# Performance work log

Measured on AMD Instinct MI355X. Metric: run time of the kernel, lower is better.

## Reference

```python
import jax, jax.numpy as jnp
import numpy as np

B, S, D = 1, 4096, 512
H, DK, DV = 8, 64, 64


def setup_inputs() -> dict:
    key = jax.random.key(0)
    ks = jax.random.split(key, 8)
    s = 1.0 / np.sqrt(D)
    return {
        "queries": jax.random.normal(ks[0], (B, S, D), jnp.float32),
        "keys": jax.random.normal(ks[1], (B, S, D), jnp.float32),
        "values": jax.random.normal(ks[2], (B, S, D), jnp.float32),
        # Linear weights stored as [in, out] for x @ W
        "Wq": jax.random.normal(ks[3], (D, H * DK), jnp.float32) * s,
        "Wk": jax.random.normal(ks[4], (D, H * DK), jnp.float32) * s,
        "Wv": jax.random.normal(ks[5], (D, H * DV), jnp.float32) * s,
        "Wo": jax.random.normal(ks[6], (H * DV, D), jnp.float32) * s,
        "bo": jax.random.normal(ks[7], (D,), jnp.float32) * 0.02,
    }


def reference(queries, keys, values, Wq, Wk, Wv, Wo, bo):
    b, qlen = values.shape[0], queries.shape[1]
    q = (queries @ Wq).reshape(b, qlen, H, DK)
    k = (keys @ Wk).reshape(b, keys.shape[1], H, DK)
    v = (values @ Wv).reshape(b, values.shape[1], H, DV)
    scale = DK ** 0.5
    # naive full attention: materialize [b, h, sq, sk] scores
    scores = jnp.einsum("bqhd,bkhd->bhqk", q, k) / scale
    attn = jax.nn.softmax(scores, axis=-1)
    out = jnp.einsum("bhqk,bkhd->bqhd", attn, v).reshape(b, qlen, H * DV)
    out = out @ Wo + bo          # first fc_out
    out = out @ Wo + bo          # second fc_out (module applies it twice when not reversible)
    return out
```

## Files before the change

kernel.cpp:

```cpp
#include <hip/hip_runtime.h>

#define S_LEN  4096
#define DMODEL 512
#define NH     8
#define HD     64

typedef _Float16 f16x8 __attribute__((ext_vector_type(8)));
typedef _Float16 f16x4 __attribute__((ext_vector_type(4)));
typedef float    f32x4 __attribute__((ext_vector_type(4)));

static __device__ __forceinline__ unsigned short f2h(float x) {
  return __builtin_bit_cast(unsigned short, (_Float16)x);
}

__global__ __launch_bounds__(256) void wtrans_kernel(
    const float* __restrict__ w0, const float* __restrict__ w1,
    const float* __restrict__ w2, const float* __restrict__ w3,
    unsigned short* __restrict__ o0, unsigned short* __restrict__ o1,
    unsigned short* __restrict__ o2, unsigned short* __restrict__ o3,
    unsigned short* __restrict__ o3s)
{
  __shared__ unsigned short T[64 * 72];
  const float* W; unsigned short* O;
  switch (blockIdx.z) {
    case 0:  W = w0; O = o0; break;
    case 1:  W = w1; O = o1; break;
    case 2:  W = w2; O = o2; break;
    default: W = w3; O = o3; break;
  }
  const int tid = threadIdx.x;
  const int k0 = blockIdx.x * 64, n0 = blockIdx.y * 64;
  const int c4 = (tid & 15) * 4;
#pragma unroll
  for (int rp = 0; rp < 4; ++rp) {
    int r = rp * 16 + (tid >> 4);
    float4 x = *(const float4*)(W + (k0 + r) * DMODEL + n0 + c4);
    T[(c4 + 0) * 72 + r] = f2h(x.x);
    T[(c4 + 1) * 72 + r] = f2h(x.y);
    T[(c4 + 2) * 72 + r] = f2h(x.z);
    T[(c4 + 3) * 72 + r] = f2h(x.w);
    if (blockIdx.z == 3) {
      f16x4 st;
      st[0] = (_Float16)x.x; st[1] = (_Float16)x.y;
      st[2] = (_Float16)x.z; st[3] = (_Float16)x.w;
      *(f16x4*)&o3s[(k0 + r) * DMODEL + n0 + c4] = st;
    }
  }
  __syncthreads();
#pragma unroll
  for (int it = 0; it < 2; ++it) {
    int i = tid + it * 256;
    int nl = i >> 3, c = i & 7;
    *(f16x8*)&O[(n0 + nl) * DMODEL + k0 + c * 8] = *(const f16x8*)&T[nl * 72 + c * 8];
  }
}

__global__ __launch_bounds__(64) void bo2_kernel(
    const float* __restrict__ Wo, const float* __restrict__ bo,
    float* __restrict__ bo2)
{
  int col = blockIdx.x * 64 + threadIdx.x;
  float s = bo[col];
#pragma unroll 8
  for (int j = 0; j < DMODEL; ++j) s = fmaf(bo[j], Wo[j * DMODEL + col], s);
  bo2[col] = s;
}

__global__ __launch_bounds__(256) void gemm_kernel(
    const void* __restrict__ A0, const void* __restrict__ A1,
    const void* __restrict__ A2, const void* __restrict__ A3,
    const unsigned short* __restrict__ B0, const unsigned short* __restrict__ B1,
    const unsigned short* __restrict__ B2, const unsigned short* __restrict__ B3,
    void* __restrict__ C0, void* __restrict__ C1,
    void* __restrict__ C2, void* __restrict__ C3,
    const float* __restrict__ bias, unsigned short* __restrict__ vtg,
    int a_fp32_mask, int c_fp32_mask)
{
  constexpr int K = DMODEL, N = DMODEL;
  __shared__ unsigned short As[64 * 32];
  __shared__ unsigned short Bs[64 * 32];
  const int z = blockIdx.z;
  if (z == 3 && blockIdx.x >= 8) return;
  const void* Av; const unsigned short* Bt; void* Cv;
  switch (z) {
    case 0:  Av = A0; Bt = B0; Cv = C0; break;
    case 1:  Av = A1; Bt = B1; Cv = C1; break;
    case 2:  Av = A2; Bt = B2; Cv = C2; break;
    default: Av = A3; Bt = B3; Cv = C3; break;
  }
  const int a_fp32 = (a_fp32_mask >> z) & 1;
  const int c_fp32 = (c_fp32_mask >> z) & 1;
  const int tid  = threadIdx.x;
  const int lane = tid & 63;
  const int wid  = tid >> 6;
  const int quad = lane >> 4, l16 = lane & 15;
  const int m0 = blockIdx.x * 64, n0 = blockIdx.y * 64;
  const int wm = (wid >> 1) * 32, wn = (wid & 1) * 32;
  const int r  = tid >> 2, ck = (tid & 3) * 8;
  f32x4 acc[2][2] = {};

  for (int k0 = 0; k0 < K; k0 += 32) {
    __syncthreads();
    if (a_fp32) {
      const float* p = (const float*)Av + (m0 + r) * K + k0 + ck;
      float4 x = *(const float4*)p;
      float4 y = *(const float4*)(p + 4);
      f16x8 av;
      av[0] = (_Float16)x.x; av[1] = (_Float16)x.y;
      av[2] = (_Float16)x.z; av[3] = (_Float16)x.w;
      av[4] = (_Float16)y.x; av[5] = (_Float16)y.y;
      av[6] = (_Float16)y.z; av[7] = (_Float16)y.w;
      *(f16x8*)&As[r * 32 + ck] = av;
    } else {
      *(f16x8*)&As[r * 32 + ck] =
          *(const f16x8*)((const unsigned short*)Av + (m0 + r) * K + k0 + ck);
    }
    *(f16x8*)&Bs[r * 32 + ck] = *(const f16x8*)(Bt + (n0 + r) * K + k0 + ck);
    __syncthreads();

    f16x8 a0 = *(const f16x8*)&As[(wm + l16) * 32 + quad * 8];
    f16x8 a1 = *(const f16x8*)&As[(wm + 16 + l16) * 32 + quad * 8];
    f16x8 b0 = *(const f16x8*)&Bs[(wn + l16) * 32 + quad * 8];
    f16x8 b1 = *(const f16x8*)&Bs[(wn + 16 + l16) * 32 + quad * 8];
    acc[0][0] = __builtin_amdgcn_mfma_f32_16x16x32_f16(a0, b0, acc[0][0], 0, 0, 0);
    acc[0][1] = __builtin_amdgcn_mfma_f32_16x16x32_f16(a0, b1, acc[0][1], 0, 0, 0);
    acc[1][0] = __builtin_amdgcn_mfma_f32_16x16x32_f16(a1, b0, acc[1][0], 0, 0, 0);
    acc[1][1] = __builtin_amdgcn_mfma_f32_16x16x32_f16(a1, b1, acc[1][1], 0, 0, 0);
  }

  const int do_vt = (vtg != nullptr) && (z == 2);
#pragma unroll
  for (int mt = 0; mt < 2; ++mt)
#pragma unroll
    for (int nt = 0; nt < 2; ++nt) {
      int col = n0 + wn + nt * 16 + l16;
      float bv = bias ? bias[col] : 0.f;
#pragma unroll
      for (int g = 0; g < 4; ++g) {
        int row = m0 + wm + mt * 16 + quad * 4 + g;
        float val = acc[mt][nt][g] + bv;
        if (do_vt)        vtg[col * S_LEN + row] = f2h(val);
        else if (c_fp32)  ((float*)Cv)[row * N + col] = val;
        else              ((unsigned short*)Cv)[row * N + col] = f2h(val);
      }
    }
}

__global__ __launch_bounds__(512) void attn_kernel(
    const unsigned short* __restrict__ Qb, const unsigned short* __restrict__ Kb,
    const unsigned short* __restrict__ VtG, unsigned short* __restrict__ Ob)
{
  __shared__ unsigned short Ks[2][64 * 72];
  __shared__ unsigned short Vt[2][64 * 72];
  __shared__ _Float16 Osc[4][64][16];
  __shared__ float    Msc[4][16];
  __shared__ float    Lsc[4][16];

  const int tid  = threadIdx.x;
  const int lane = tid & 63;
  const int wid  = tid >> 6;
  const int qsub = wid & 3;
  const int kh   = wid >> 2;
  const int quad = lane >> 4, l16 = lane & 15;
  const int qb = blockIdx.x, h = blockIdx.y;
  const int hc = h * HD;

  const int qrow = qb * 64 + qsub * 16 + l16;
  const f16x8 bq0 = *(const f16x8*)(Qb + qrow * DMODEL + hc + quad * 8);
  const f16x8 bq1 = *(const f16x8*)(Qb + qrow * DMODEL + hc + 32 + quad * 8);

  f32x4 o[4] = {};
  float m_run = -1e30f, l_run = 0.f;

  for (int kbi = 0; kbi < 32; ++kbi) {
    __syncthreads();
#pragma unroll
    for (int it = 0; it < 2; ++it) {
      int s = it * 512 + tid;
      int khs = s >> 9, n = (s >> 3) & 63, c = s & 7;
      int key = khs * 2048 + kbi * 64 + n;
      *(f16x8*)&Ks[khs][n * 72 + c * 8] =
          *(const f16x8*)(Kb + key * DMODEL + hc + c * 8);
      *(f16x8*)&Vt[khs][n * 72 + c * 8] =
          *(const f16x8*)(VtG + (hc + n) * S_LEN + khs * 2048 + kbi * 64 + c * 8);
    }
    __syncthreads();

    f32x4 sT[4];
#pragma unroll
    for (int kt = 0; kt < 4; ++kt) {
      f32x4 a = {};
      f16x8 ak0 = *(const f16x8*)&Ks[kh][(kt * 16 + l16) * 72 + quad * 8];
      f16x8 ak1 = *(const f16x8*)&Ks[kh][(kt * 16 + l16) * 72 + 32 + quad * 8];
      a = __builtin_amdgcn_mfma_f32_16x16x32_f16(ak0, bq0, a, 0, 0, 0);
      a = __builtin_amdgcn_mfma_f32_16x16x32_f16(ak1, bq1, a, 0, 0, 0);
      sT[kt] = a;
    }

    float vmax = -1e30f;
#pragma unroll
    for (int kt = 0; kt < 4; ++kt)
#pragma unroll
      for (int g = 0; g < 4; ++g) vmax = fmaxf(vmax, sT[kt][g]);
    vmax = fmaxf(vmax, __shfl_xor(vmax, 16));
    vmax = fmaxf(vmax, __shfl_xor(vmax, 32));
    const float mn = fmaxf(m_run, vmax);
    const float alpha = __expf((m_run - mn) * 0.125f);
    m_run = mn;

    float rs = 0.f;
    f16x4 pa[4];
#pragma unroll
    for (int kt = 0; kt < 4; ++kt)
#pragma unroll
      for (int g = 0; g < 4; ++g) {
        float p = __expf((sT[kt][g] - mn) * 0.125f);
        rs += p;
        pa[kt][g] = (_Float16)p;
      }
    rs += __shfl_xor(rs, 16);
    rs += __shfl_xor(rs, 32);
    l_run = l_run * alpha + rs;

    float ag[4];
#pragma unroll
    for (int g = 0; g < 4; ++g) ag[g] = __shfl(alpha, quad * 4 + g);
#pragma unroll
    for (int nt = 0; nt < 4; ++nt)
#pragma unroll
      for (int g = 0; g < 4; ++g) o[nt][g] *= ag[g];

#pragma unroll
    for (int nt = 0; nt < 4; ++nt)
#pragma unroll
      for (int kt = 0; kt < 4; ++kt) {
        f16x4 bv = *(const f16x4*)&Vt[kh][(nt * 16 + l16) * 72 + kt * 16 + quad * 4];
        o[nt] = __builtin_amdgcn_mfma_f32_16x16x16f16(pa[kt], bv, o[nt], 0, 0, 0);
      }
  }

  __syncthreads();
  if (kh == 1) {
    if (quad == 0) { Msc[qsub][l16] = m_run; Lsc[qsub][l16] = l_run; }
#pragma unroll
    for (int nt = 0; nt < 4; ++nt)
#pragma unroll
      for (int g = 0; g < 4; ++g)
        Osc[qsub][lane][nt * 4 + g] = (_Float16)o[nt][g];
  }
  __syncthreads();
  if (kh == 0) {
    const float m1 = Msc[qsub][l16];
    const float l1 = Lsc[qsub][l16];
    const float m  = fmaxf(m_run, m1);
    const float a0 = __expf((m_run - m) * 0.125f);
    const float a1 = __expf((m1 - m) * 0.125f);
    const float rl = 1.f / (l_run * a0 + l1 * a1);
    float a0g[4], a1g[4], rlg[4];
#pragma unroll
    for (int g = 0; g < 4; ++g) {
      a0g[g] = __shfl(a0, quad * 4 + g);
      a1g[g] = __shfl(a1, quad * 4 + g);
      rlg[g] = __shfl(rl, quad * 4 + g);
    }
#pragma unroll
    for (int g = 0; g < 4; ++g) {
      int row = qb * 64 + qsub * 16 + quad * 4 + g;
#pragma unroll
      for (int nt = 0; nt < 4; ++nt) {
        float om = o[nt][g] * a0g[g] + (float)Osc[qsub][lane][nt * 4 + g] * a1g[g];
        Ob[row * DMODEL + hc + nt * 16 + l16] = f2h(om * rlg[g]);
      }
    }
  }
}

extern "C" void kernel_launch(void* const* d_in, const int* in_sizes, int n_in,
                              void* d_out, int out_size, void* d_ws, size_t ws_size,
                              hipStream_t stream) {
  const float* q  = (const float*)d_in[0];
  const float* k  = (const float*)d_in[1];
  const float* v  = (const float*)d_in[2];
  const float* Wq = (const float*)d_in[3];
  const float* Wk = (const float*)d_in[4];
  const float* Wv = (const float*)d_in[5];
  const float* Wo = (const float*)d_in[6];
  const float* bo = (const float*)d_in[7];

  unsigned short* ws   = (unsigned short*)d_ws;
  unsigned short* Wqt  = ws;
  unsigned short* Wkt  = Wqt  + 262144;
  unsigned short* Wvt  = Wkt  + 262144;
  unsigned short* Wot  = Wvt  + 262144;
  unsigned short* Wof  = Wot  + 262144;
  unsigned short* Wo2t = Wof  + 262144;
  unsigned short* Qb   = Wo2t + 262144;
  unsigned short* Kb   = Qb   + 2097152;
  unsigned short* VtG  = Kb   + 2097152;
  unsigned short* Ab   = VtG  + 2097152;
  float*          bo2  = (float*)(Ab + 2097152);

  wtrans_kernel<<<dim3(8, 8, 4), 256, 0, stream>>>(
      Wq, Wk, Wv, Wo, Wqt, Wkt, Wvt, Wot, Wof);

  bo2_kernel<<<dim3(8), 64, 0, stream>>>(Wo, bo, bo2);

  gemm_kernel<<<dim3(64, 8, 4), 256, 0, stream>>>(
      q, k, v, Wot, Wqt, Wkt, Wvt, Wof, Qb, Kb, nullptr, Wo2t,
      nullptr, VtG, 0x7, 0x0);

  attn_kernel<<<dim3(64, 8), 512, 0, stream>>>(Qb, Kb, VtG, Ab);

  gemm_kernel<<<dim3(64, 8, 1), 256, 0, stream>>>(
      Ab, nullptr, nullptr, nullptr, Wo2t, nullptr, nullptr, nullptr,
      d_out, nullptr, nullptr, nullptr, bo2, nullptr, 0x0, 0x1);
}
```

Before: 214.4 us.

## Process two query subtiles per wave in attention and fold bias kernel into GEMM

The attention kernel now gives each wave 32 query rows (two 16-row subtiles) instead of 16. Each block covers 128 queries and the grid is halved, so every K/V tile staged in shared memory is reused by twice as many queries, halving global K/V traffic and the per-tile load and sync overhead. The separate bo2 bias-precompute kernel is removed and its work runs in otherwise idle blocks of the first GEMM launch, saving one launch. The cost is more registers per wave and half as many blocks (256), which may reduce occupancy and latency hiding on a GPU with many CUs.

```diff
diff --git a/kernel.cpp b/kernel.cpp
--- a/kernel.cpp
+++ b/kernel.cpp
@@ -55,17 +55,6 @@
   }
 }
 
-__global__ __launch_bounds__(64) void bo2_kernel(
-    const float* __restrict__ Wo, const float* __restrict__ bo,
-    float* __restrict__ bo2)
-{
-  int col = blockIdx.x * 64 + threadIdx.x;
-  float s = bo[col];
-#pragma unroll 8
-  for (int j = 0; j < DMODEL; ++j) s = fmaf(bo[j], Wo[j * DMODEL + col], s);
-  bo2[col] = s;
-}
-
 __global__ __launch_bounds__(256) void gemm_kernel(
     const void* __restrict__ A0, const void* __restrict__ A1,
     const void* __restrict__ A2, const void* __restrict__ A3,
@@ -74,13 +63,24 @@
     void* __restrict__ C0, void* __restrict__ C1,
     void* __restrict__ C2, void* __restrict__ C3,
     const float* __restrict__ bias, unsigned short* __restrict__ vtg,
+    const float* __restrict__ wo_f32, const float* __restrict__ bo_in,
+    float* __restrict__ bo2_out,
     int a_fp32_mask, int c_fp32_mask)
 {
   constexpr int K = DMODEL, N = DMODEL;
   __shared__ unsigned short As[64 * 32];
   __shared__ unsigned short Bs[64 * 32];
   const int z = blockIdx.z;
-  if (z == 3 && blockIdx.x >= 8) return;
+  if (z == 3 && blockIdx.x >= 8) {
+    if (blockIdx.x < 16 && blockIdx.y == 0 && wo_f32) {
+      int col = (blockIdx.x - 8) * 64 + (threadIdx.x & 63);
+      float s = bo_in[col];
+#pragma unroll 8
+      for (int j = 0; j < DMODEL; ++j) s = fmaf(bo_in[j], wo_f32[j * DMODEL + col], s);
+      bo2_out[col] = s;
+    }
+    return;
+  }
   const void* Av; const unsigned short* Bt; void* Cv;
   switch (z) {
     case 0:  Av = A0; Bt = B0; Cv = C0; break;
@@ -152,25 +152,30 @@
 {
   __shared__ unsigned short Ks[2][64 * 72];
   __shared__ unsigned short Vt[2][64 * 72];
-  __shared__ _Float16 Osc[4][64][16];
-  __shared__ float    Msc[4][16];
-  __shared__ float    Lsc[4][16];
+  __shared__ _Float16 Osc[4][64][32];
+  __shared__ float    Msc[4][2][16];
+  __shared__ float    Lsc[4][2][16];
 
   const int tid  = threadIdx.x;
   const int lane = tid & 63;
   const int wid  = tid >> 6;
-  const int qsub = wid & 3;
+  const int qp   = wid & 3;
   const int kh   = wid >> 2;
   const int quad = lane >> 4, l16 = lane & 15;
   const int qb = blockIdx.x, h = blockIdx.y;
   const int hc = h * HD;
-
-  const int qrow = qb * 64 + qsub * 16 + l16;
-  const f16x8 bq0 = *(const f16x8*)(Qb + qrow * DMODEL + hc + quad * 8);
-  const f16x8 bq1 = *(const f16x8*)(Qb + qrow * DMODEL + hc + 32 + quad * 8);
-
-  f32x4 o[4] = {};
-  float m_run = -1e30f, l_run = 0.f;
+  const int qbase = qb * 128 + qp * 32;
+
+  f16x8 bq[2][2];
+#pragma unroll
+  for (int s = 0; s < 2; ++s) {
+    int qrow = qbase + s * 16 + l16;
+    bq[s][0] = *(const f16x8*)(Qb + qrow * DMODEL + hc + quad * 8);
+    bq[s][1] = *(const f16x8*)(Qb + qrow * DMODEL + hc + 32 + quad * 8);
+  }
+
+  f32x4 o[2][4] = {};
+  float m_run[2] = {-1e30f, -1e30f}, l_run[2] = {0.f, 0.f};
 
   for (int kbi = 0; kbi < 32; ++kbi) {
     __syncthreads();
@@ -186,90 +191,104 @@
     }
     __syncthreads();
 
-    f32x4 sT[4];
+    f32x4 sT[2][4];
 #pragma unroll
     for (int kt = 0; kt < 4; ++kt) {
-      f32x4 a = {};
       f16x8 ak0 = *(const f16x8*)&Ks[kh][(kt * 16 + l16) * 72 + quad * 8];
       f16x8 ak1 = *(const f16x8*)&Ks[kh][(kt * 16 + l16) * 72 + 32 + quad * 8];
-      a = __builtin_amdgcn_mfma_f32_16x16x32_f16(ak0, bq0, a, 0, 0, 0);
-      a = __builtin_amdgcn_mfma_f32_16x16x32_f16(ak1, bq1, a, 0, 0, 0);
-      sT[kt] = a;
-    }
-
-    float vmax = -1e30f;
-#pragma unroll
-    for (int kt = 0; kt < 4; ++kt)
-#pragma unroll
-      for (int g = 0; g < 4; ++g) vmax = fmaxf(vmax, sT[kt][g]);
-    vmax = fmaxf(vmax, __shfl_xor(vmax, 16));
-    vmax = fmaxf(vmax, __shfl_xor(vmax, 32));
-    const float mn = fmaxf(m_run, vmax);
-    const float alpha = __expf((m_run - mn) * 0.125f);
-    m_run = mn;
-
-    float rs = 0.f;
-    f16x4 pa[4];
-#pragma unroll
-    for (int kt = 0; kt < 4; ++kt)
-#pragma unroll
-      for (int g = 0; g < 4; ++g) {
-        float p = __expf((sT[kt][g] - mn) * 0.125f);
-        rs += p;
-        pa[kt][g] = (_Float16)p;
-      }
-    rs += __shfl_xor(rs, 16);
-    rs += __shfl_xor(rs, 32);
-    l_run = l_run * alpha + rs;
-
-    float ag[4];
-#pragma unroll
-    for (int g = 0; g < 4; ++g) ag[g] = __shfl(alpha, quad * 4 + g);
-#pragma unroll
-    for (int nt = 0; nt < 4; ++nt)
-#pragma unroll
-      for (int g = 0; g < 4; ++g) o[nt][g] *= ag[g];
+#pragma unroll
+      for (int s = 0; s < 2; ++s) {
+        f32x4 a = {};
+        a = __builtin_amdgcn_mfma_f32_16x16x32_f16(ak0, bq[s][0], a, 0, 0, 0);
+        a = __builtin_amdgcn_mfma_f32_16x16x32_f16(ak1, bq[s][1], a, 0, 0, 0);
+        sT[s][kt] = a;
+      }
+    }
+
+    f16x4 pa[2][4];
+#pragma unroll
+    for (int s = 0; s < 2; ++s) {
+      float vmax = -1e30f;
+#pragma unroll
+      for (int kt = 0; kt < 4; ++kt)
+#pragma unroll
+        for (int g = 0; g < 4; ++g) vmax = fmaxf(vmax, sT[s][kt][g]);
+      vmax = fmaxf(vmax, __shfl_xor(vmax, 16));
+      vmax = fmaxf(vmax, __shfl_xor(vmax, 32));
+      const float mn = fmaxf(m_run[s], vmax);
+      const float alpha = __expf((m_run[s] - mn) * 0.125f);
+      m_run[s] = mn;
+
+      float rs = 0.f;
+#pragma unroll
+      for (int kt = 0; kt < 4; ++kt)
+#pragma unroll
+        for (int g = 0; g < 4; ++g) {
+          float p = __expf((sT[s][kt][g] - mn) * 0.125f);
+          rs += p;
+          pa[s][kt][g] = (_Float16)p;
+        }
+      rs += __shfl_xor(rs, 16);
+      rs += __shfl_xor(rs, 32);
+      l_run[s] = l_run[s] * alpha + rs;
+
+      float ag[4];
+#pragma unroll
+      for (int g = 0; g < 4; ++g) ag[g] = __shfl(alpha, quad * 4 + g);
+#pragma unroll
+      for (int nt = 0; nt < 4; ++nt)
+#pragma unroll
+        for (int g = 0; g < 4; ++g) o[s][nt][g] *= ag[g];
+    }
 
 #pragma unroll
     for (int nt = 0; nt < 4; ++nt)
 #pragma unroll
       for (int kt = 0; kt < 4; ++kt) {
         f16x4 bv = *(const f16x4*)&Vt[kh][(nt * 16 + l16) * 72 + kt * 16 + quad * 4];
-        o[nt] = __builtin_amdgcn_mfma_f32_16x16x16f16(pa[kt], bv, o[nt], 0, 0, 0);
+#pragma unroll
+        for (int s = 0; s < 2; ++s)
+          o[s][nt] = __builtin_amdgcn_mfma_f32_16x16x16f16(pa[s][kt], bv, o[s][nt], 0, 0, 0);
       }
   }
 
   __syncthreads();
   if (kh == 1) {
-    if (quad == 0) { Msc[qsub][l16] = m_run; Lsc[qsub][l16] = l_run; }
-#pragma unroll
-    for (int nt = 0; nt < 4; ++nt)
-#pragma unroll
-      for (int g = 0; g < 4; ++g)
-        Osc[qsub][lane][nt * 4 + g] = (_Float16)o[nt][g];
+#pragma unroll
+    for (int s = 0; s < 2; ++s) {
+      if (quad == 0) { Msc[qp][s][l16] = m_run[s]; Lsc[qp][s][l16] = l_run[s]; }
+#pragma unroll
+      for (int nt = 0; nt < 4; ++nt)
+#pragma unroll
+        for (int g = 0; g < 4; ++g)
+          Osc[qp][lane][s * 16 + nt * 4 + g] = (_Float16)o[s][nt][g];
+    }
   }
   __syncthreads();
   if (kh == 0) {
-    const float m1 = Msc[qsub][l16];
-    const float l1 = Lsc[qsub][l16];
-    const float m  = fmaxf(m_run, m1);
-    const float a0 = __expf((m_run - m) * 0.125f);
-    const float a1 = __expf((m1 - m) * 0.125f);
-    const float rl = 1.f / (l_run * a0 + l1 * a1);
-    float a0g[4], a1g[4], rlg[4];
-#pragma unroll
-    for (int g = 0; g < 4; ++g) {
-      a0g[g] = __shfl(a0, quad * 4 + g);
-      a1g[g] = __shfl(a1, quad * 4 + g);
-      rlg[g] = __shfl(rl, quad * 4 + g);
-    }
-#pragma unroll
-    for (int g = 0; g < 4; ++g) {
-      int row = qb * 64 + qsub * 16 + quad * 4 + g;
-#pragma unroll
-      for (int nt = 0; nt < 4; ++nt) {
-        float om = o[nt][g] * a0g[g] + (float)Osc[qsub][lane][nt * 4 + g] * a1g[g];
-        Ob[row * DMODEL + hc + nt * 16 + l16] = f2h(om * rlg[g]);
+#pragma unroll
+    for (int s = 0; s < 2; ++s) {
+      const float m1 = Msc[qp][s][l16];
+      const float l1 = Lsc[qp][s][l16];
+      const float m  = fmaxf(m_run[s], m1);
+      const float a0 = __expf((m_run[s] - m) * 0.125f);
+      const float a1 = __expf((m1 - m) * 0.125f);
+      const float rl = 1.f / (l_run[s] * a0 + l1 * a1);
+      float a0g[4], a1g[4], rlg[4];
+#pragma unroll
+      for (int g = 0; g < 4; ++g) {
+        a0g[g] = __shfl(a0, quad * 4 + g);
+        a1g[g] = __shfl(a1, quad * 4 + g);
+        rlg[g] = __shfl(rl, quad * 4 + g);
+      }
+#pragma unroll
+      for (int g = 0; g < 4; ++g) {
+        int row = qbase + s * 16 + quad * 4 + g;
+#pragma unroll
+        for (int nt = 0; nt < 4; ++nt) {
+          float om = o[s][nt][g] * a0g[g] + (float)Osc[qp][lane][s * 16 + nt * 4 + g] * a1g[g];
+          Ob[row * DMODEL + hc + nt * 16 + l16] = f2h(om * rlg[g]);
+        }
       }
     }
   }
@@ -303,15 +322,14 @@
   wtrans_kernel<<<dim3(8, 8, 4), 256, 0, stream>>>(
       Wq, Wk, Wv, Wo, Wqt, Wkt, Wvt, Wot, Wof);
 
-  bo2_kernel<<<dim3(8), 64, 0, stream>>>(Wo, bo, bo2);
-
   gemm_kernel<<<dim3(64, 8, 4), 256, 0, stream>>>(
       q, k, v, Wot, Wqt, Wkt, Wvt, Wof, Qb, Kb, nullptr, Wo2t,
-      nullptr, VtG, 0x7, 0x0);
-
-  attn_kernel<<<dim3(64, 8), 512, 0, stream>>>(Qb, Kb, VtG, Ab);
+      nullptr, VtG, Wo, bo, bo2, 0x7, 0x0);
+
+  attn_kernel<<<dim3(32, 8), 512, 0, stream>>>(Qb, Kb, VtG, Ab);
 
   gemm_kernel<<<dim3(64, 8, 1), 256, 0, stream>>>(
       Ab, nullptr, nullptr, nullptr, Wo2t, nullptr, nullptr, nullptr,
-      d_out, nullptr, nullptr, nullptr, bo2, nullptr, 0x0, 0x1);
-}
+      d_out, nullptr, nullptr, nullptr, bo2, nullptr,
+      nullptr, nullptr, nullptr, 0x0, 0x1);
+}
```

Result: faster. 204.9 us (-4.4%).
